# Optimization experiments

Measured on AMD Instinct MI355X. Metric: run time of the kernel, lower is better.

Reference implementation:

```python
import jax, jax.numpy as jnp
import numpy as np

B, C, H, W = 4, 256, 64, 64
CK = C // 8   # 32, theta/phi channels
CV = C // 2   # 128, g channels


def setup_inputs() -> dict:
    key = jax.random.key(0)
    ks = jax.random.split(key, 10)
    s = lambda fan: 1.0 / np.sqrt(fan)
    inp = {
        "x": jax.random.normal(ks[0], (B, C, H, W), dtype=jnp.float32),
        "theta_w": jax.random.normal(ks[1], (CK, C), dtype=jnp.float32) * s(C),
        "theta_b": jax.random.normal(ks[2], (CK,), dtype=jnp.float32) * 0.01,
        "phi_w": jax.random.normal(ks[3], (CK, C), dtype=jnp.float32) * s(C),
        "phi_b": jax.random.normal(ks[4], (CK,), dtype=jnp.float32) * 0.01,
        "g_w": jax.random.normal(ks[5], (CV, C), dtype=jnp.float32) * s(C),
        "g_b": jax.random.normal(ks[6], (CV,), dtype=jnp.float32) * 0.01,
        "o_w": jax.random.normal(ks[7], (C, CV), dtype=jnp.float32) * s(CV),
        "o_b": jax.random.normal(ks[8], (C,), dtype=jnp.float32) * 0.01,
        "gamma": jax.random.normal(ks[9], (1,), dtype=jnp.float32) * 0.1,
    }
    return inp


def reference(x, theta_w, theta_b, phi_w, phi_b, g_w, g_b, o_w, o_b, gamma):
    b, c, h, w = x.shape
    n = h * w
    xf = x.reshape(b, c, n)  # [B, C, N]
    # 1x1 convs == per-pixel linear projections
    theta = jnp.einsum('oc,bcn->bon', theta_w, xf) + theta_b[None, :, None]  # [B, CK, N]
    phi = jnp.einsum('oc,bcn->bon', phi_w, xf) + phi_b[None, :, None]        # [B, CK, N]
    g = jnp.einsum('oc,bcn->bon', g_w, xf) + g_b[None, :, None]              # [B, CV, N]
    # scores[b, i, j] = theta_i . phi_j ; softmax over dim=1 (query axis i) as in torch code
    scores = jnp.einsum('bci,bcj->bij', theta, phi)  # [B, N, N]
    attention = jax.nn.softmax(scores, axis=1)
    # o_pre = bmm(g, attention^T): o_pre[b, c, i] = sum_j g[b, c, j] * attention[b, i, j]
    o_pre = jnp.einsum('bcj,bij->bci', g, attention)  # [B, CV, N]
    o = jnp.einsum('oc,bcn->bon', o_w, o_pre) + o_b[None, :, None]  # [B, C, N]
    out = (gamma[0] * o + xf).reshape(b, c, h, w)
    return out
```

## Files before the change

kernel.cpp:

```cpp
#include <hip/hip_runtime.h>
#include <math.h>

#define B_  4
#define C_  256
#define N_  4096
#define CK_ 32
#define CV_ 128

typedef __attribute__((ext_vector_type(8))) short short8;
typedef __attribute__((ext_vector_type(4))) float f32x4;
typedef unsigned short u16;
typedef unsigned int   u32;

static constexpr float LOG2E = 1.4426950408889634f;

static __device__ __forceinline__ u16 f2bf(float f) {
    u32 u = __float_as_uint(f);
    u = (u + 0x7FFFu + ((u >> 16) & 1u)) >> 16;
    return (u16)u;
}
static __device__ __forceinline__ float bf2f(u16 h) {
    return __uint_as_float(((u32)h) << 16);
}

static __device__ __forceinline__ float fexp2(float x) {
#if __has_builtin(__builtin_amdgcn_exp2f)
    return __builtin_amdgcn_exp2f(x);
#else
    float r; asm("v_exp_f32 %0, %1\n\ts_nop 0" : "=v"(r) : "v"(x)); return r;
#endif
}
static __device__ __forceinline__ float frcp(float x) {
#if __has_builtin(__builtin_amdgcn_rcpf)
    return __builtin_amdgcn_rcpf(x);
#else
    float r; asm("v_rcp_f32 %0, %1\n\ts_nop 0" : "=v"(r) : "v"(x)); return r;
#endif
}
static __device__ __forceinline__ u32 cvt_pk_bf16(float a, float b) {
    u32 r; asm("v_cvt_pk_bf16_f32 %0, %1, %2" : "=v"(r) : "v"(a), "v"(b));
    return r;
}

__global__ __launch_bounds__(256) void prep_kernel(
    const float* __restrict__ x, u16* __restrict__ xT16,
    const float* __restrict__ theta_w, const float* __restrict__ phi_w,
    const float* __restrict__ g_w,     const float* __restrict__ o_w,
    u16* __restrict__ W16, u16* __restrict__ ow16)
{
    if (blockIdx.x >= N_ / 64) {
        const int base = (((blockIdx.x - N_ / 64) * 16 + blockIdx.y * 4 + blockIdx.z) * 256
                          + threadIdx.x) * 4;
        #pragma unroll
        for (int e0 = 0; e0 < 4; ++e0) {
            const int e = base + e0;
            if (e < 8192)        W16[e] = f2bf(theta_w[e] * LOG2E);
            else if (e < 16384)  W16[e] = f2bf(phi_w[e - 8192]);
            else if (e < 49152)  W16[e] = f2bf(g_w[e - 16384]);
            else                 ow16[e - 49152] = f2bf(o_w[e - 49152]);
        }
        return;
    }

    const int b = blockIdx.z, c0 = blockIdx.y * 64, n0 = blockIdx.x * 64;
    const int t = threadIdx.x;
    __shared__ float tile[64][65];

    const int cr = t >> 4, nc = (t & 15) * 4;
    #pragma unroll
    for (int it = 0; it < 4; ++it) {
        const float4 v = *(const float4*)(x + (size_t)(b * C_ + c0 + cr + it * 16) * N_ + n0 + nc);
        tile[cr + it * 16][nc + 0] = v.x; tile[cr + it * 16][nc + 1] = v.y;
        tile[cr + it * 16][nc + 2] = v.z; tile[cr + it * 16][nc + 3] = v.w;
    }
    __syncthreads();
    const int n = t >> 2, cg = (t & 3) * 16;
    union { u16 us[16]; uint4 u4[2]; } pk;
    #pragma unroll
    for (int e = 0; e < 16; ++e) pk.us[e] = f2bf(tile[cg + e][n]);
    uint4* dst = (uint4*)(xT16 + (size_t)(b * N_ + n0 + n) * C_ + c0 + cg);
    dst[0] = pk.u4[0]; dst[1] = pk.u4[1];
}

__global__ __launch_bounds__(256) void proj_mfma_kernel(
    const u16* __restrict__ xT16, const u16* __restrict__ W16,
    const float* __restrict__ theta_b, const float* __restrict__ phi_b,
    const float* __restrict__ g_b,
    u16* __restrict__ theta_t, u16* __restrict__ phi_t, u16* __restrict__ g2)
{
    const int b = blockIdx.y, n0 = blockIdx.x * 64;
    const int w = threadIdx.x >> 6, lane = threadIdx.x & 63;
    const int lr = lane & 15, q = lane >> 4;
    const f32x4 zf = {0.f, 0.f, 0.f, 0.f};

    const u16* xrow = xT16 + (size_t)(b * N_ + n0 + w * 16 + lr) * C_;
    f32x4 acc[4];
    #pragma unroll
    for (int nt = 0; nt < 4; ++nt) acc[nt] = zf;
    for (int ks = 0; ks < 8; ++ks) {
        const short8 aX = *(const short8*)(xrow + ks * 32 + q * 8);
        #pragma unroll
        for (int nt = 0; nt < 4; ++nt) {
            const short8 bW = *(const short8*)(W16 + (size_t)(nt * 16 + lr) * C_ + ks * 32 + q * 8);
            acc[nt] = __builtin_amdgcn_mfma_f32_16x16x32_bf16(aX, bW, acc[nt], 0, 0, 0);
        }
    }
    #pragma unroll
    for (int nt = 0; nt < 4; ++nt) {
        const int o = nt * 16 + lr;
        #pragma unroll
        for (int reg = 0; reg < 4; ++reg) {
            const int n = n0 + w * 16 + q * 4 + reg;
            if (nt < 2)
                theta_t[(size_t)(b * N_ + n) * CK_ + o] = f2bf(acc[nt][reg] + theta_b[o] * LOG2E);
            else
                phi_t[(size_t)(b * N_ + n) * CK_ + (o - 32)] = f2bf(acc[nt][reg] + phi_b[o - 32]);
        }
    }

    #pragma unroll
    for (int mp = 0; mp < 2; ++mp) {
        const int ctile = w * 2 + mp;
        const int crow = ctile * 16;
        f32x4 ag[4];
        #pragma unroll
        for (int nt = 0; nt < 4; ++nt) ag[nt] = zf;
        for (int ks = 0; ks < 8; ++ks) {
            const short8 aW = *(const short8*)(W16 + (size_t)(64 + crow + lr) * C_ + ks * 32 + q * 8);
            #pragma unroll
            for (int nt = 0; nt < 4; ++nt) {
                const short8 bX = *(const short8*)(xT16 + (size_t)(b * N_ + n0 + nt * 16 + lr) * C_ + ks * 32 + q * 8);
                ag[nt] = __builtin_amdgcn_mfma_f32_16x16x32_bf16(aW, bX, ag[nt], 0, 0, 0);
            }
        }
        #pragma unroll
        for (int nt = 0; nt < 4; ++nt) {
            const int jchunk = (n0 >> 5) + (nt >> 1);
            const int lhi = (nt & 1) * 2 + (lr >> 3);
            #pragma unroll
            for (int reg = 0; reg < 4; ++reg) {
                const int c = crow + q * 4 + reg;
                const int lane2 = (q * 4 + reg) + 16 * lhi;
                g2[((size_t)(b * 8 + ctile) * 128 + jchunk) * 512 + lane2 * 8 + (lr & 7)]
                    = f2bf(ag[nt][reg] + g_b[c]);
            }
        }
    }
}

__global__ __launch_bounds__(256) void colstats_kernel(
    const u16* __restrict__ theta_t, const u16* __restrict__ phi_t,
    float* __restrict__ Z)
{
    const int b  = blockIdx.z;
    const int j0 = blockIdx.x * 32;
    const int istart = blockIdx.y * (N_ / 4);
    const int tid = threadIdx.x;
    const int wave = tid >> 6, lane = tid & 63;
    const int lr = lane & 15, q = lane >> 4;

    const int jW = j0 + (wave & 1) * 16;
    const short8 bF = *(const short8*)(phi_t + (size_t)(b * N_ + jW + lr) * CK_ + q * 8);

    const u16* thp = theta_t + (size_t)b * N_ * CK_;
    const f32x4 zero = {0.f, 0.f, 0.f, 0.f};
    float zacc = 0.f;
    for (int it = istart + (wave >> 1) * 16; it < istart + N_ / 4; it += 32) {
        const short8 aF = *(const short8*)(thp + (size_t)(it + lr) * CK_ + q * 8);
        f32x4 S = __builtin_amdgcn_mfma_f32_16x16x32_bf16(aF, bF, zero, 0, 0, 0);
        zacc += fexp2(S[0]) + fexp2(S[1]) + fexp2(S[2]) + fexp2(S[3]);
    }
    zacc += __shfl_xor(zacc, 16);
    zacc += __shfl_xor(zacc, 32);
    if (lane < 16) atomicAdd(&Z[(size_t)b * N_ + jW + lr], zacc);
}

__global__ __launch_bounds__(256) void gscale_kernel(
    u16* __restrict__ g2, const float* __restrict__ Z)
{
    const size_t idx = ((size_t)blockIdx.x * 256 + threadIdx.x) * 8;
    const int b = (int)(idx >> 19);
    const int j = (int)(((idx >> 9) & 127) * 32 + ((idx >> 7) & 3) * 8);
    uint4 raw = *(const uint4*)(g2 + idx);
    const float4 z0 = *(const float4*)(Z + (size_t)b * N_ + j);
    const float4 z1 = *(const float4*)(Z + (size_t)b * N_ + j + 4);
    const float zz[8] = {z0.x, z0.y, z0.z, z0.w, z1.x, z1.y, z1.z, z1.w};
    u16* pr = (u16*)&raw;
    union { u16 us[8]; uint4 u4; } pk;
    #pragma unroll
    for (int k = 0; k < 8; ++k) pk.us[k] = f2bf(bf2f(pr[k]) * frcp(zz[k]));
    *(uint4*)(g2 + idx) = pk.u4;
}

__global__ __launch_bounds__(256, 1) void opre_kernel(
    const u16* __restrict__ theta_t, const u16* __restrict__ phi_t,
    const u16* __restrict__ g2,
    float* __restrict__ o_p0, float* __restrict__ o_p1)
{
    const int bx = blockIdx.x;
    const int igg = bx & 7, ch = (bx >> 3) & 3, jh = (bx >> 5) & 1, b = bx >> 6;
    const int w = threadIdx.x >> 6, lane = threadIdx.x & 63;
    const int lr = lane & 15, q = lane >> 4;
    const int i0 = (igg * 4 + w) * 128;
    const f32x4 zf = {0.f, 0.f, 0.f, 0.f};

    short8 bT[8];
    #pragma unroll
    for (int it = 0; it < 8; ++it)
        bT[it] = *(const short8*)(theta_t + (size_t)(b * N_ + i0 + it * 16 + lr) * CK_ + q * 8);

    const int ja = (lr >> 2) * 8 + (lr & 3);
    const int jstart = jh * (N_ / 2);
    const u16* pA = phi_t + ((size_t)(b * N_) + jstart + ja) * CK_ + q * 8;
    const u16* pG = g2 + ((size_t)(b * 8 + ch * 2) * 128 + jh * 64) * 512 + lane * 8;

    f32x4 acc[8][2];
    #pragma unroll
    for (int it = 0; it < 8; ++it) { acc[it][0] = zf; acc[it][1] = zf; }

    short8 A0a = *(const short8*)(pA);
    short8 A1a = *(const short8*)(pA + 4 * CK_);
    short8 G0a = *(const short8*)(pG);
    short8 G1a = *(const short8*)(pG + 128 * 512);
    short8 A0b = *(const short8*)(pA + 32 * CK_);
    short8 A1b = *(const short8*)(pA + 36 * CK_);
    short8 G0b = *(const short8*)(pG + 512);
    short8 G1b = *(const short8*)(pG + 128 * 512 + 512);

#define OPRE_CHUNK(K, A0r, A1r, G0r, G1r)                                          \
    {                                                                               \
        const short8 cA0 = A0r, cA1 = A1r, cG0 = G0r, cG1 = G1r;                    \
        const int kn = ((K) + 2) & 63;                                              \
        A0r = *(const short8*)(pA + (size_t)kn * (32 * CK_));                       \
        A1r = *(const short8*)(pA + (size_t)kn * (32 * CK_) + 4 * CK_);             \
        G0r = *(const short8*)(pG + kn * 512);                                      \
        G1r = *(const short8*)(pG + 128 * 512 + kn * 512);                          \
        _Pragma("unroll")                                                           \
        for (int it = 0; it < 8; ++it) {                                            \
            const f32x4 Sa = __builtin_amdgcn_mfma_f32_16x16x32_bf16(cA0, bT[it], zf, 0, 0, 0); \
            const f32x4 Sb = __builtin_amdgcn_mfma_f32_16x16x32_bf16(cA1, bT[it], zf, 0, 0, 0); \
            union { u32 u[4]; short8 s8; } ef;                                      \
            ef.u[0] = cvt_pk_bf16(fexp2(Sa[0]), fexp2(Sa[1]));                      \
            ef.u[1] = cvt_pk_bf16(fexp2(Sa[2]), fexp2(Sa[3]));                      \
            ef.u[2] = cvt_pk_bf16(fexp2(Sb[0]), fexp2(Sb[1]));                      \
            ef.u[3] = cvt_pk_bf16(fexp2(Sb[2]), fexp2(Sb[3]));                      \
            acc[it][0] = __builtin_amdgcn_mfma_f32_16x16x32_bf16(ef.s8, cG0, acc[it][0], 0, 0, 0); \
            acc[it][1] = __builtin_amdgcn_mfma_f32_16x16x32_bf16(ef.s8, cG1, acc[it][1], 0, 0, 0); \
        }                                                                           \
    }

    for (int k = 0; k < 64; k += 2) {
        OPRE_CHUNK(k,     A0a, A1a, G0a, G1a)
        OPRE_CHUNK(k + 1, A0b, A1b, G0b, G1b)
    }
#undef OPRE_CHUNK

    float* op = (jh ? o_p1 : o_p0);
    #pragma unroll
    for (int it = 0; it < 8; ++it) {
        const size_t tb = ((size_t)(b * 256 + (i0 >> 4) + it) * 4 + ch) * 512;
        #pragma unroll
        for (int ct = 0; ct < 2; ++ct) {
            #pragma unroll
            for (int reg = 0; reg < 4; ++reg) {
                const int lane2 = (q * 4 + reg) + 16 * (ct * 2 + (lr >> 3));
                op[tb + lane2 * 8 + (lr & 7)] = acc[it][ct][reg];
            }
        }
    }
}

__global__ __launch_bounds__(256) void final_mfma_kernel(
    const float* __restrict__ o_p0, const float* __restrict__ o_p1,
    const u16* __restrict__ ow16, const float* __restrict__ o_b,
    const float* __restrict__ gamma, const float* __restrict__ x,
    float* __restrict__ out)
{
    const int b = blockIdx.y, n0 = blockIdx.x * 32;
    const int w = threadIdx.x >> 6, lane = threadIdx.x & 63;
    const int lr = lane & 15, q = lane >> 4;
    const f32x4 zf = {0.f, 0.f, 0.f, 0.f};

    f32x4 acc[4][2];
    #pragma unroll
    for (int mt = 0; mt < 4; ++mt)
        #pragma unroll
        for (int nt = 0; nt < 2; ++nt) acc[mt][nt] = zf;

    for (int ks = 0; ks < 4; ++ks) {
        short8 bP[2];
        #pragma unroll
        for (int nt = 0; nt < 2; ++nt) {
            const size_t base = (((size_t)(b * 256 + (n0 >> 4) + nt) * 4 + ks) * 64 + lane) * 8;
            const float4 a0 = *(const float4*)(o_p0 + base);
            const float4 a1 = *(const float4*)(o_p0 + base + 4);
            const float4 c0 = *(const float4*)(o_p1 + base);
            const float4 c1 = *(const float4*)(o_p1 + base + 4);
            union { u32 u[4]; short8 s8; } pk;
            pk.u[0] = cvt_pk_bf16(a0.x + c0.x, a0.y + c0.y);
            pk.u[1] = cvt_pk_bf16(a0.z + c0.z, a0.w + c0.w);
            pk.u[2] = cvt_pk_bf16(a1.x + c1.x, a1.y + c1.y);
            pk.u[3] = cvt_pk_bf16(a1.z + c1.z, a1.w + c1.w);
            bP[nt] = pk.s8;
        }
        #pragma unroll
        for (int mt = 0; mt < 4; ++mt) {
            const short8 aW = *(const short8*)(ow16 + (size_t)((w * 4 + mt) * 16 + lr) * CV_ + ks * 32 + q * 8);
            #pragma unroll
            for (int nt = 0; nt < 2; ++nt)
                acc[mt][nt] = __builtin_amdgcn_mfma_f32_16x16x32_bf16(aW, bP[nt], acc[mt][nt], 0, 0, 0);
        }
    }

    const float gm = gamma[0];
    #pragma unroll
    for (int mt = 0; mt < 4; ++mt) {
        #pragma unroll
        for (int nt = 0; nt < 2; ++nt) {
            #pragma unroll
            for (int reg = 0; reg < 4; ++reg) {
                const int oc = (w * 4 + mt) * 16 + q * 4 + reg;
                const int n = n0 + nt * 16 + lr;
                const size_t off = (size_t)(b * C_ + oc) * N_ + n;
                out[off] = x[off] + gm * (acc[mt][nt][reg] + o_b[oc]);
            }
        }
    }
}

extern "C" void kernel_launch(void* const* d_in, const int* in_sizes, int n_in,
                              void* d_out, int out_size, void* d_ws, size_t ws_size,
                              hipStream_t stream)
{
    const float* x       = (const float*)d_in[0];
    const float* theta_w = (const float*)d_in[1];
    const float* theta_b = (const float*)d_in[2];
    const float* phi_w   = (const float*)d_in[3];
    const float* phi_b   = (const float*)d_in[4];
    const float* g_w     = (const float*)d_in[5];
    const float* g_b     = (const float*)d_in[6];
    const float* o_w     = (const float*)d_in[7];
    const float* o_b     = (const float*)d_in[8];
    const float* gamma   = (const float*)d_in[9];
    float* out = (float*)d_out;

    u16* xT16    = (u16*)d_ws;
    u16* W16     = xT16 + (size_t)B_ * N_ * C_;
    u16* ow16    = W16 + 192 * C_;
    u16* theta_t = ow16 + C_ * CV_;
    u16* phi_t   = theta_t + (size_t)B_ * N_ * CK_;
    u16* g2      = phi_t + (size_t)B_ * N_ * CK_;
    float* Z     = (float*)(g2 + (size_t)B_ * CV_ * N_);
    float* o_p0  = Z + (size_t)B_ * N_;
    float* o_p1  = o_p0 + (size_t)B_ * N_ * CV_;

    hipMemsetAsync(Z, 0, (size_t)B_ * N_ * sizeof(float), stream);

    prep_kernel<<<dim3(N_ / 64 + 5, C_ / 64, B_), 256, 0, stream>>>(
        x, xT16, theta_w, phi_w, g_w, o_w, W16, ow16);
    proj_mfma_kernel<<<dim3(N_ / 64, B_), 256, 0, stream>>>(
        xT16, W16, theta_b, phi_b, g_b, theta_t, phi_t, g2);
    colstats_kernel<<<dim3(N_ / 32, 4, B_), 256, 0, stream>>>(theta_t, phi_t, Z);
    gscale_kernel<<<dim3((B_ * CV_ * N_) / 2048), 256, 0, stream>>>(g2, Z);
    opre_kernel<<<dim3(256), 256, 0, stream>>>(theta_t, phi_t, g2, o_p0, o_p1);
    final_mfma_kernel<<<dim3(N_ / 32, B_), 256, 0, stream>>>(
        o_p0, o_p1, ow16, o_b, gamma, x, out);
}
```

Baseline: 200.4 us.

## Split opre key dimension into four partitions to double grid parallelism

The attention-output kernel now splits the key (j) axis four ways instead of two, launching 512 blocks rather than 256 so that more of the GPU's compute units are busy. The two extra partial sums are written as bf16 into the reused xT16 workspace, and the final kernel reads and sums all four partials. This trades extra partial-sum traffic and some bf16 rounding of partials for better occupancy of the dominant kernel.

```diff
diff --git a/kernel.cpp b/kernel.cpp
--- a/kernel.cpp
+++ b/kernel.cpp
@@ -195,10 +195,10 @@
 __global__ __launch_bounds__(256, 1) void opre_kernel(
     const u16* __restrict__ theta_t, const u16* __restrict__ phi_t,
     const u16* __restrict__ g2,
-    float* __restrict__ o_p0, float* __restrict__ o_p1)
+    float* __restrict__ o_p0, float* __restrict__ o_p1, u16* __restrict__ opb)
 {
     const int bx = blockIdx.x;
-    const int igg = bx & 7, ch = (bx >> 3) & 3, jh = (bx >> 5) & 1, b = bx >> 6;
+    const int igg = bx & 7, ch = (bx >> 3) & 3, jq = (bx >> 5) & 3, b = bx >> 7;
     const int w = threadIdx.x >> 6, lane = threadIdx.x & 63;
     const int lr = lane & 15, q = lane >> 4;
     const int i0 = (igg * 4 + w) * 128;
@@ -210,9 +210,9 @@
         bT[it] = *(const short8*)(theta_t + (size_t)(b * N_ + i0 + it * 16 + lr) * CK_ + q * 8);
 
     const int ja = (lr >> 2) * 8 + (lr & 3);
-    const int jstart = jh * (N_ / 2);
+    const int jstart = jq * (N_ / 4);
     const u16* pA = phi_t + ((size_t)(b * N_) + jstart + ja) * CK_ + q * 8;
-    const u16* pG = g2 + ((size_t)(b * 8 + ch * 2) * 128 + jh * 64) * 512 + lane * 8;
+    const u16* pG = g2 + ((size_t)(b * 8 + ch * 2) * 128 + jq * 32) * 512 + lane * 8;
 
     f32x4 acc[8][2];
     #pragma unroll
@@ -230,7 +230,7 @@
 #define OPRE_CHUNK(K, A0r, A1r, G0r, G1r)                                          \
     {                                                                               \
         const short8 cA0 = A0r, cA1 = A1r, cG0 = G0r, cG1 = G1r;                    \
-        const int kn = ((K) + 2) & 63;                                              \
+        const int kn = ((K) + 2) & 31;                                              \
         A0r = *(const short8*)(pA + (size_t)kn * (32 * CK_));                       \
         A1r = *(const short8*)(pA + (size_t)kn * (32 * CK_) + 4 * CK_);             \
         G0r = *(const short8*)(pG + kn * 512);                                      \
@@ -249,22 +249,38 @@
         }                                                                           \
     }
 
-    for (int k = 0; k < 64; k += 2) {
+    for (int k = 0; k < 32; k += 2) {
         OPRE_CHUNK(k,     A0a, A1a, G0a, G1a)
         OPRE_CHUNK(k + 1, A0b, A1b, G0b, G1b)
     }
 #undef OPRE_CHUNK
 
-    float* op = (jh ? o_p1 : o_p0);
-    #pragma unroll
-    for (int it = 0; it < 8; ++it) {
-        const size_t tb = ((size_t)(b * 256 + (i0 >> 4) + it) * 4 + ch) * 512;
-        #pragma unroll
-        for (int ct = 0; ct < 2; ++ct) {
-            #pragma unroll
-            for (int reg = 0; reg < 4; ++reg) {
-                const int lane2 = (q * 4 + reg) + 16 * (ct * 2 + (lr >> 3));
-                op[tb + lane2 * 8 + (lr & 7)] = acc[it][ct][reg];
+    if (jq < 2) {
+        float* op = (jq ? o_p1 : o_p0);
+        #pragma unroll
+        for (int it = 0; it < 8; ++it) {
+            const size_t tb = ((size_t)(b * 256 + (i0 >> 4) + it) * 4 + ch) * 512;
+            #pragma unroll
+            for (int ct = 0; ct < 2; ++ct) {
+                #pragma unroll
+                for (int reg = 0; reg < 4; ++reg) {
+                    const int lane2 = (q * 4 + reg) + 16 * (ct * 2 + (lr >> 3));
+                    op[tb + lane2 * 8 + (lr & 7)] = acc[it][ct][reg];
+                }
+            }
+        }
+    } else {
+        u16* ob = opb + (size_t)(jq - 2) * ((size_t)B_ * N_ * CV_);
+        #pragma unroll
+        for (int it = 0; it < 8; ++it) {
+            const size_t tb = ((size_t)(b * 256 + (i0 >> 4) + it) * 4 + ch) * 512;
+            #pragma unroll
+            for (int ct = 0; ct < 2; ++ct) {
+                #pragma unroll
+                for (int reg = 0; reg < 4; ++reg) {
+                    const int lane2 = (q * 4 + reg) + 16 * (ct * 2 + (lr >> 3));
+                    ob[tb + lane2 * 8 + (lr & 7)] = f2bf(acc[it][ct][reg]);
+                }
             }
         }
     }
@@ -272,6 +288,7 @@
 
 __global__ __launch_bounds__(256) void final_mfma_kernel(
     const float* __restrict__ o_p0, const float* __restrict__ o_p1,
+    const u16* __restrict__ opb,
     const u16* __restrict__ ow16, const float* __restrict__ o_b,
     const float* __restrict__ gamma, const float* __restrict__ x,
     float* __restrict__ out)
@@ -280,6 +297,7 @@
     const int w = threadIdx.x >> 6, lane = threadIdx.x & 63;
     const int lr = lane & 15, q = lane >> 4;
     const f32x4 zf = {0.f, 0.f, 0.f, 0.f};
+    const size_t QS = (size_t)B_ * N_ * CV_;
 
     f32x4 acc[4][2];
     #pragma unroll
@@ -296,11 +314,19 @@
             const float4 a1 = *(const float4*)(o_p0 + base + 4);
             const float4 c0 = *(const float4*)(o_p1 + base);
             const float4 c1 = *(const float4*)(o_p1 + base + 4);
+            union { u16 us[8]; uint4 u4; } w2, w3;
+            w2.u4 = *(const uint4*)(opb + base);
+            w3.u4 = *(const uint4*)(opb + QS + base);
+            float s[8] = {a0.x + c0.x, a0.y + c0.y, a0.z + c0.z, a0.w + c0.w,
+                          a1.x + c1.x, a1.y + c1.y, a1.z + c1.z, a1.w + c1.w};
+            #pragma unroll
+            for (int e = 0; e < 8; ++e)
+                s[e] += bf2f(w2.us[e]) + bf2f(w3.us[e]);
             union { u32 u[4]; short8 s8; } pk;
-            pk.u[0] = cvt_pk_bf16(a0.x + c0.x, a0.y + c0.y);
-            pk.u[1] = cvt_pk_bf16(a0.z + c0.z, a0.w + c0.w);
-            pk.u[2] = cvt_pk_bf16(a1.x + c1.x, a1.y + c1.y);
-            pk.u[3] = cvt_pk_bf16(a1.z + c1.z, a1.w + c1.w);
+            pk.u[0] = cvt_pk_bf16(s[0], s[1]);
+            pk.u[1] = cvt_pk_bf16(s[2], s[3]);
+            pk.u[2] = cvt_pk_bf16(s[4], s[5]);
+            pk.u[3] = cvt_pk_bf16(s[6], s[7]);
             bP[nt] = pk.s8;
         }
         #pragma unroll
@@ -353,6 +379,7 @@
     float* Z     = (float*)(g2 + (size_t)B_ * CV_ * N_);
     float* o_p0  = Z + (size_t)B_ * N_;
     float* o_p1  = o_p0 + (size_t)B_ * N_ * CV_;
+    u16* opb     = xT16;
 
     hipMemsetAsync(Z, 0, (size_t)B_ * N_ * sizeof(float), stream);
 
@@ -362,7 +389,7 @@
         xT16, W16, theta_b, phi_b, g_b, theta_t, phi_t, g2);
     colstats_kernel<<<dim3(N_ / 32, 4, B_), 256, 0, stream>>>(theta_t, phi_t, Z);
     gscale_kernel<<<dim3((B_ * CV_ * N_) / 2048), 256, 0, stream>>>(g2, Z);
-    opre_kernel<<<dim3(256), 256, 0, stream>>>(theta_t, phi_t, g2, o_p0, o_p1);
+    opre_kernel<<<dim3(512), 256, 0, stream>>>(theta_t, phi_t, g2, o_p0, o_p1, opb);
     final_mfma_kernel<<<dim3(N_ / 32, B_), 256, 0, stream>>>(
-        o_p0, o_p1, ow16, o_b, gamma, x, out);
-}
+        o_p0, o_p1, opb, ow16, o_b, gamma, x, out);
+}
```

Measured after the change: 193.7 us. 3.4% less time.
